# Kernel tuning notes

Hardware: AMD Instinct MI355X
Metric: run time of the kernel (lower is better)

Reference implementation:

```python
import jax, jax.numpy as jnp
import numpy as np

NUM_HEADS = 16

def rotate_half(x):
    h = x.shape[-1] // 2
    return jnp.concatenate([-x[..., h:], x[..., :h]], axis=-1)

def setup_inputs() -> dict:
    key = jax.random.key(0)
    ks = jax.random.split(key, 6)
    B, S, D, HD = 2, 2048, 2048, 128
    x = jax.random.normal(ks[0], (B, S, D), dtype=jnp.float32)
    # rotary tables for positions 0..S-1, per head_dim channel
    inv_freq = 1.0 / (10000.0 ** (jnp.arange(0, HD, 2, dtype=jnp.float32) / HD))
    t = jnp.arange(S, dtype=jnp.float32)
    freqs = jnp.outer(t, inv_freq)              # [S, HD/2]
    emb = jnp.concatenate([freqs, freqs], -1)   # [S, HD]
    cos = jnp.cos(emb)
    sin = jnp.sin(emb)
    scale = 0.02
    qkv_w = jax.random.normal(ks[1], (D, 3 * D), dtype=jnp.float32) * scale
    qkv_b = jnp.zeros((3 * D,), dtype=jnp.float32)
    out_w = jax.random.normal(ks[2], (D, D), dtype=jnp.float32) * scale
    out_b = jnp.zeros((D,), dtype=jnp.float32)
    return {"x": x, "cos": cos, "sin": sin, "qkv_w": qkv_w, "qkv_b": qkv_b,
            "out_w": out_w, "out_b": out_b}

def reference(x, cos, sin, qkv_w, qkv_b, out_w, out_b):
    B, S, D = x.shape
    H = NUM_HEADS
    HD = D // H
    qkv = x @ qkv_w + qkv_b                      # [B,S,3D]
    q, k, v = jnp.split(qkv, 3, axis=-1)
    def to_heads(t):
        return t.reshape(B, S, H, HD).transpose(0, 2, 1, 3)  # [B,H,S,HD]
    q, k, v = to_heads(q), to_heads(k), to_heads(v)
    # RoPE: cos/sin are [S,HD], broadcast over batch/head
    q = q * cos + rotate_half(q) * sin
    k = k * cos + rotate_half(k) * sin
    scores = jnp.einsum('bhqd,bhkd->bhqk', q, k) / jnp.sqrt(jnp.float32(HD))
    causal = jnp.tril(jnp.ones((S, S), dtype=bool))
    scores = jnp.where(causal, scores, jnp.finfo(scores.dtype).min)
    attn = jax.nn.softmax(scores, axis=-1)
    out = jnp.einsum('bhqk,bhkd->bhqd', attn, v)  # [B,H,S,HD]
    out = out.transpose(0, 2, 1, 3).reshape(B, S, D)
    return out @ out_w + out_b
```

## Files before the change

### kernel.cpp

```cpp
#include <hip/hip_runtime.h>
#include <cstddef>
#include <cstdint>

typedef __attribute__((ext_vector_type(8))) short bh8_t;
typedef __attribute__((ext_vector_type(4))) float f4_t;

__device__ __forceinline__ unsigned short f2bf(float x) {
    union { float f; unsigned u; } v; v.f = x;
    unsigned r = v.u + 0x7fffu + ((v.u >> 16) & 1u);
    return (unsigned short)(r >> 16);
}
__device__ __forceinline__ float bf2f(unsigned short u) {
    union { unsigned u; float f; } v; v.u = ((unsigned)u) << 16;
    return v.f;
}

__device__ __forceinline__ void gl_lds16(const void* g, void* l) {
    __builtin_amdgcn_global_load_lds(
        (const __attribute__((address_space(1))) unsigned int*)g,
        (__attribute__((address_space(3))) unsigned int*)l, 16, 0, 0);
}

#define B_    2
#define S_    2048
#define D_    2048
#define H_    16
#define HD_   128

__global__ __launch_bounds__(256) void cvt_f32_bf16(const float* __restrict__ in,
                                                    ushort* __restrict__ out) {
    size_t i = ((size_t)blockIdx.x * 256 + threadIdx.x) * 8;
    float4 a = *(const float4*)&in[i];
    float4 b = *(const float4*)&in[i + 4];
    ushort4 o0, o1;
    o0.x = f2bf(a.x); o0.y = f2bf(a.y); o0.z = f2bf(a.z); o0.w = f2bf(a.w);
    o1.x = f2bf(b.x); o1.y = f2bf(b.y); o1.z = f2bf(b.z); o1.w = f2bf(b.w);
    *(ushort4*)&out[i]     = o0;
    *(ushort4*)&out[i + 4] = o1;
}

__global__ __launch_bounds__(256) void transp_f32_bf16(const float* __restrict__ in,
                                                       ushort* __restrict__ out,
                                                       int R, int C) {
    __shared__ float T[64][68];
    const int t = threadIdx.x, rl = t >> 4, cl = t & 15;
    const int r0 = blockIdx.y * 64, c0 = blockIdx.x * 64;
    #pragma unroll
    for (int j = 0; j < 4; ++j) {
        int row = rl + 16 * j;
        float4 v = *(const float4*)&in[(size_t)(r0 + row) * C + c0 + cl * 4];
        *(float4*)&T[row][cl * 4] = v;
    }
    __syncthreads();
    #pragma unroll
    for (int j = 0; j < 4; ++j) {
        int row = rl + 16 * j;
        ushort4 o;
        o.x = f2bf(T[cl * 4 + 0][row]);
        o.y = f2bf(T[cl * 4 + 1][row]);
        o.z = f2bf(T[cl * 4 + 2][row]);
        o.w = f2bf(T[cl * 4 + 3][row]);
        *(ushort4*)&out[(size_t)(c0 + row) * R + r0 + cl * 4] = o;
    }
}

__global__ __launch_bounds__(256) void qkv_gemm(const ushort* __restrict__ A,
                                                const ushort* __restrict__ Bt,
                                                const float* __restrict__ bias,
                                                ushort* __restrict__ Qb,
                                                ushort* __restrict__ Kb,
                                                ushort* __restrict__ Vtg) {
    __shared__ ushort Al[2][128 * 32];
    __shared__ ushort Bl[2][128 * 32];
    const int tid = threadIdx.x;
    const int l = tid & 63, wv = tid >> 6;
    const int lr = l & 15, bk = l >> 4;
    const int wr = wv >> 1, wc = wv & 1;
    const int row0 = blockIdx.x * 128, col0 = blockIdx.y * 128;

    f4_t zero4 = {0.f, 0.f, 0.f, 0.f};
    f4_t acc[4][4];
    #pragma unroll
    for (int i = 0; i < 4; ++i)
        #pragma unroll
        for (int j = 0; j < 4; ++j) acc[i][j] = zero4;

    const int c0 = tid, c1 = tid + 256;
    const ushort* Ap0 = A  + (size_t)(row0 + (c0 >> 2)) * 2048 + (c0 & 3) * 8;
    const ushort* Ap1 = A  + (size_t)(row0 + (c1 >> 2)) * 2048 + (c1 & 3) * 8;
    const ushort* Bp0 = Bt + (size_t)(col0 + (c0 >> 2)) * 2048 + (c0 & 3) * 8;
    const ushort* Bp1 = Bt + (size_t)(col0 + (c1 >> 2)) * 2048 + (c1 & 3) * 8;
    const int d0 = (c0 - l) * 8, d1 = (c1 - l) * 8;

    auto issue = [&](int k0, int buf) {
        gl_lds16(Ap0 + k0, &Al[buf][d0]);
        gl_lds16(Ap1 + k0, &Al[buf][d1]);
        gl_lds16(Bp0 + k0, &Bl[buf][d0]);
        gl_lds16(Bp1 + k0, &Bl[buf][d1]);
    };

    issue(0, 0);
    for (int k0 = 0; k0 < 2048; k0 += 32) {
        const int buf = (k0 >> 5) & 1;
        if (k0 + 32 < 2048) {
            issue(k0 + 32, buf ^ 1);
            asm volatile("s_waitcnt vmcnt(4)" ::: "memory");
        } else {
            asm volatile("s_waitcnt vmcnt(0)" ::: "memory");
        }
        __builtin_amdgcn_s_barrier();
        asm volatile("" ::: "memory");
        bh8_t af[4], bf[4];
        #pragma unroll
        for (int mf = 0; mf < 4; ++mf)
            af[mf] = *(const bh8_t*)&Al[buf][(wr * 64 + mf * 16 + lr) * 32 + bk * 8];
        #pragma unroll
        for (int nf = 0; nf < 4; ++nf)
            bf[nf] = *(const bh8_t*)&Bl[buf][(wc * 64 + nf * 16 + lr) * 32 + bk * 8];
        __builtin_amdgcn_s_setprio(1);
        #pragma unroll
        for (int mf = 0; mf < 4; ++mf)
            #pragma unroll
            for (int nf = 0; nf < 4; ++nf)
                acc[mf][nf] = __builtin_amdgcn_mfma_f32_16x16x32_bf16(
                    af[mf], bf[nf], acc[mf][nf], 0, 0, 0);
        __builtin_amdgcn_s_setprio(0);
        asm volatile("" ::: "memory");
        __builtin_amdgcn_s_barrier();
        asm volatile("" ::: "memory");
    }

    const int which = col0 >> 11;
    const int h = (col0 & 2047) >> 7;
    if (which < 2) {
        ushort* dst = which == 0 ? Qb : Kb;
        #pragma unroll
        for (int nf = 0; nf < 4; ++nf) {
            int n = col0 + wc * 64 + nf * 16 + lr;
            float bv = bias[n];
            int hd = (n & 2047) & 127;
            #pragma unroll
            for (int mf = 0; mf < 4; ++mf) {
                int mbase = row0 + wr * 64 + mf * 16 + bk * 4;
                #pragma unroll
                for (int r = 0; r < 4; ++r) {
                    int m = mbase + r;
                    int b = m >> 11, s = m & 2047;
                    dst[((size_t)(b * 16 + h) * 2048 + s) * 128 + hd] =
                        f2bf(acc[mf][nf][r] + bv);
                }
            }
        }
    } else {
        #pragma unroll
        for (int nf = 0; nf < 4; ++nf) {
            int n = col0 + wc * 64 + nf * 16 + lr;
            float bv = bias[n];
            int hd = n & 127;
            #pragma unroll
            for (int mf = 0; mf < 4; ++mf) {
                int mbase = row0 + wr * 64 + mf * 16 + bk * 4;
                int b = mbase >> 11, s4 = mbase & 2047;
                int spos = (s4 & ~31) | (((s4 >> 2) & 3) << 3) | (((s4 >> 4) & 1) << 2);
                ushort4 o;
                o.x = f2bf(acc[mf][nf][0] + bv);
                o.y = f2bf(acc[mf][nf][1] + bv);
                o.z = f2bf(acc[mf][nf][2] + bv);
                o.w = f2bf(acc[mf][nf][3] + bv);
                *(ushort4*)&Vtg[((size_t)((b * 16 + h) * 128 + hd)) * 2048 + spos] = o;
            }
        }
    }
}

__global__ __launch_bounds__(256) void rope_bf16(ushort* __restrict__ Qb,
                                                 ushort* __restrict__ Kb,
                                                 const float* __restrict__ cosn,
                                                 const float* __restrict__ sinn) {
    unsigned idx = blockIdx.x * 256 + threadIdx.x;
    int regn = idx >> 20;
    unsigned rest = idx & 1048575u;
    unsigned row = rest >> 4;
    int g = rest & 15;
    int s = row & 2047;
    ushort* base = (regn ? Kb : Qb) + (size_t)row * 128 + g * 4;
    uint2 lo = *(const uint2*)base;
    uint2 hi = *(const uint2*)(base + 64);
    float4 c4 = *(const float4*)&cosn[s * 128 + g * 4];
    float4 s4 = *(const float4*)&sinn[s * 128 + g * 4];
    const float sc = regn ? 1.0f : 0.08838834764831845f;
    const ushort* lp = (const ushort*)&lo;
    const ushort* hp = (const ushort*)&hi;
    float cf[4] = {c4.x, c4.y, c4.z, c4.w};
    float sf[4] = {s4.x, s4.y, s4.z, s4.w};
    ushort4 olo, ohi;
    ushort* olp = (ushort*)&olo;
    ushort* ohp = (ushort*)&ohi;
    #pragma unroll
    for (int e = 0; e < 4; ++e) {
        float lv = bf2f(lp[e]), hv = bf2f(hp[e]);
        olp[e] = f2bf((lv * cf[e] - hv * sf[e]) * sc);
        ohp[e] = f2bf((hv * cf[e] + lv * sf[e]) * sc);
    }
    *(ushort4*)base        = olo;
    *(ushort4*)(base + 64) = ohi;
}

__global__ __launch_bounds__(512) void attn3(const ushort* __restrict__ Qb,
                                             const ushort* __restrict__ Kb,
                                             const ushort* __restrict__ Vtg,
                                             ushort* __restrict__ AO) {
    __shared__ ushort lds[2][16384];
    const int tid = threadIdx.x;
    const int l = tid & 63, wq = tid >> 6;
    const int lr = l & 15, bk = l >> 4;
    const int id = blockIdx.x;
    const int bh = id & 31;
    const int qb2 = 15 - (id >> 5);
    const int q0 = qb2 * 128;
    const int qrow = q0 + wq * 16 + lr;
    const ushort* Qg = Qb + ((size_t)bh * 2048 + qrow) * 128;
    const ushort* KgB = Kb + (size_t)bh * 2048 * 128;
    const ushort* VgB = Vtg + (size_t)bh * 128 * 2048;

    bh8_t qf[4];
    #pragma unroll
    for (int ks = 0; ks < 4; ++ks)
        qf[ks] = *(const bh8_t*)(Qg + ks * 32 + bk * 8);

    float mrun = -1e30f, lrun = 0.f;
    f4_t zero4 = {0.f, 0.f, 0.f, 0.f};
    f4_t oacc[8];
    #pragma unroll
    for (int i = 0; i < 8; ++i) oacc[i] = zero4;

    auto issue = [&](int kt, int buf) {
        ushort* Kl = &lds[buf][0];
        ushort* Vl = &lds[buf][8192];
        const ushort* Kg = KgB + (size_t)kt * 64 * 128;
        #pragma unroll
        for (int i = 0; i < 2; ++i) {
            int c = tid + 512 * i;
            int key = c >> 4, d8 = (c & 15) ^ (key & 7);
            gl_lds16(Kg + key * 128 + d8 * 8, Kl + (size_t)(c - l) * 8);
        }
        #pragma unroll
        for (int i = 0; i < 2; ++i) {
            int c = tid + 512 * i;
            int d = c >> 3, p8 = (c & 7) ^ (d & 7);
            gl_lds16(VgB + (size_t)d * 2048 + kt * 64 + p8 * 8,
                     Vl + (size_t)(c - l) * 8);
        }
    };

    const int nkt = 2 * qb2 + 2;
    issue(0, 0);
    for (int kt = 0; kt < nkt; ++kt) {
        const int buf = kt & 1;
        if (kt + 1 < nkt) {
            issue(kt + 1, buf ^ 1);
            asm volatile("s_waitcnt vmcnt(4)" ::: "memory");
        } else {
            asm volatile("s_waitcnt vmcnt(0)" ::: "memory");
        }
        __builtin_amdgcn_s_barrier();
        asm volatile("" ::: "memory");

        if (kt * 64 <= q0 + wq * 16 + 15) {
            const char* Kl = (const char*)&lds[buf][0];
            const char* Vl = (const char*)&lds[buf][8192];

            f4_t sacc[4];
            #pragma unroll
            for (int kf = 0; kf < 4; ++kf) sacc[kf] = zero4;
            __builtin_amdgcn_s_setprio(1);
            #pragma unroll
            for (int ks = 0; ks < 4; ++ks)
                #pragma unroll
                for (int kf = 0; kf < 4; ++kf) {
                    int key = kf * 16 + lr;
                    int ab = (key * 256 + ks * 64 + bk * 16) ^ ((key & 7) << 4);
                    bh8_t kv = *(const bh8_t*)(Kl + ab);
                    sacc[kf] = __builtin_amdgcn_mfma_f32_16x16x32_bf16(
                        kv, qf[ks], sacc[kf], 0, 0, 0);
                }
            __builtin_amdgcn_s_setprio(0);

            if (kt * 64 + 63 > q0 + wq * 16) {
                #pragma unroll
                for (int kf = 0; kf < 4; ++kf)
                    #pragma unroll
                    for (int r = 0; r < 4; ++r) {
                        int key = kt * 64 + kf * 16 + bk * 4 + r;
                        if (key > qrow) sacc[kf][r] = -1e30f;
                    }
            }
            float mt = -1e30f;
            #pragma unroll
            for (int kf = 0; kf < 4; ++kf)
                #pragma unroll
                for (int r = 0; r < 4; ++r) mt = fmaxf(mt, sacc[kf][r]);
            mt = fmaxf(mt, __shfl_xor(mt, 16));
            mt = fmaxf(mt, __shfl_xor(mt, 32));
            float mnew = fmaxf(mrun, mt);
            float alpha = __expf(mrun - mnew);
            float rsum = 0.f;
            #pragma unroll
            for (int kf = 0; kf < 4; ++kf)
                #pragma unroll
                for (int r = 0; r < 4; ++r) {
                    float p = __expf(sacc[kf][r] - mnew);
                    sacc[kf][r] = p;
                    rsum += p;
                }
            rsum += __shfl_xor(rsum, 16);
            rsum += __shfl_xor(rsum, 32);
            lrun = lrun * alpha + rsum;
            mrun = mnew;
            #pragma unroll
            for (int df = 0; df < 8; ++df) oacc[df] *= alpha;

            union { unsigned u[4]; bh8_t v; } bop[2];
            #pragma unroll
            for (int ks2 = 0; ks2 < 2; ++ks2)
                #pragma unroll
                for (int e = 0; e < 8; e += 2) {
                    unsigned lo16 = f2bf(sacc[2 * ks2 + (e >> 2)][e & 3]);
                    unsigned hi16 = f2bf(sacc[2 * ks2 + ((e + 1) >> 2)][(e + 1) & 3]);
                    bop[ks2].u[e >> 1] = lo16 | (hi16 << 16);
                }
            __builtin_amdgcn_s_setprio(1);
            #pragma unroll
            for (int df = 0; df < 8; ++df) {
                int d = df * 16 + lr;
                #pragma unroll
                for (int ks2 = 0; ks2 < 2; ++ks2) {
                    int ab = (d * 128 + ks2 * 64 + bk * 16) ^ ((d & 7) << 4);
                    bh8_t av = *(const bh8_t*)(Vl + ab);
                    oacc[df] = __builtin_amdgcn_mfma_f32_16x16x32_bf16(
                        av, bop[ks2].v, oacc[df], 0, 0, 0);
                }
            }
            __builtin_amdgcn_s_setprio(0);
        }
        asm volatile("" ::: "memory");
        __builtin_amdgcn_s_barrier();
        asm volatile("" ::: "memory");
    }

    float inv = 1.0f / lrun;
    const int b = bh >> 4, h = bh & 15;
    #pragma unroll
    for (int df = 0; df < 8; ++df) {
        ushort4 o;
        o.x = f2bf(oacc[df][0] * inv);
        o.y = f2bf(oacc[df][1] * inv);
        o.z = f2bf(oacc[df][2] * inv);
        o.w = f2bf(oacc[df][3] * inv);
        size_t off = ((size_t)(b * 2048 + qrow)) * 2048 + h * 128 + df * 16 + bk * 4;
        *(ushort4*)&AO[off] = o;
    }
}

__global__ __launch_bounds__(256) void out_gemm(const ushort* __restrict__ A,
                                                const ushort* __restrict__ Bt,
                                                const float* __restrict__ bias,
                                                float* __restrict__ out) {
    __shared__ ushort Al[2][128 * 32];
    __shared__ ushort Bl[2][128 * 32];
    const int tid = threadIdx.x;
    const int l = tid & 63, wv = tid >> 6;
    const int lr = l & 15, bk = l >> 4;
    const int wr = wv >> 1, wc = wv & 1;
    const int row0 = blockIdx.x * 128, col0 = blockIdx.y * 128;

    f4_t zero4 = {0.f, 0.f, 0.f, 0.f};
    f4_t acc[4][4];
    #pragma unroll
    for (int i = 0; i < 4; ++i)
        #pragma unroll
        for (int j = 0; j < 4; ++j) acc[i][j] = zero4;

    const int c0 = tid, c1 = tid + 256;
    const ushort* Ap0 = A  + (size_t)(row0 + (c0 >> 2)) * 2048 + (c0 & 3) * 8;
    const ushort* Ap1 = A  + (size_t)(row0 + (c1 >> 2)) * 2048 + (c1 & 3) * 8;
    const ushort* Bp0 = Bt + (size_t)(col0 + (c0 >> 2)) * 2048 + (c0 & 3) * 8;
    const ushort* Bp1 = Bt + (size_t)(col0 + (c1 >> 2)) * 2048 + (c1 & 3) * 8;
    const int d0 = (c0 - l) * 8, d1 = (c1 - l) * 8;

    auto issue = [&](int k0, int buf) {
        gl_lds16(Ap0 + k0, &Al[buf][d0]);
        gl_lds16(Ap1 + k0, &Al[buf][d1]);
        gl_lds16(Bp0 + k0, &Bl[buf][d0]);
        gl_lds16(Bp1 + k0, &Bl[buf][d1]);
    };

    issue(0, 0);
    for (int k0 = 0; k0 < 2048; k0 += 32) {
        const int buf = (k0 >> 5) & 1;
        if (k0 + 32 < 2048) {
            issue(k0 + 32, buf ^ 1);
            asm volatile("s_waitcnt vmcnt(4)" ::: "memory");
        } else {
            asm volatile("s_waitcnt vmcnt(0)" ::: "memory");
        }
        __builtin_amdgcn_s_barrier();
        asm volatile("" ::: "memory");
        bh8_t af[4], bf[4];
        #pragma unroll
        for (int mf = 0; mf < 4; ++mf)
            af[mf] = *(const bh8_t*)&Al[buf][(wr * 64 + mf * 16 + lr) * 32 + bk * 8];
        #pragma unroll
        for (int nf = 0; nf < 4; ++nf)
            bf[nf] = *(const bh8_t*)&Bl[buf][(wc * 64 + nf * 16 + lr) * 32 + bk * 8];
        __builtin_amdgcn_s_setprio(1);
        #pragma unroll
        for (int mf = 0; mf < 4; ++mf)
            #pragma unroll
            for (int nf = 0; nf < 4; ++nf)
                acc[mf][nf] = __builtin_amdgcn_mfma_f32_16x16x32_bf16(
                    af[mf], bf[nf], acc[mf][nf], 0, 0, 0);
        __builtin_amdgcn_s_setprio(0);
        asm volatile("" ::: "memory");
        __builtin_amdgcn_s_barrier();
        asm volatile("" ::: "memory");
    }

    #pragma unroll
    for (int nf = 0; nf < 4; ++nf) {
        int n = col0 + wc * 64 + nf * 16 + lr;
        float bv = bias[n];
        #pragma unroll
        for (int mf = 0; mf < 4; ++mf) {
            int mbase = row0 + wr * 64 + mf * 16 + bk * 4;
            #pragma unroll
            for (int r = 0; r < 4; ++r)
                out[(size_t)(mbase + r) * 2048 + n] = acc[mf][nf][r] + bv;
        }
    }
}

extern "C" void kernel_launch(void* const* d_in, const int* in_sizes, int n_in,
                              void* d_out, int out_size, void* d_ws, size_t ws_size,
                              hipStream_t stream)
{
    (void)in_sizes; (void)n_in; (void)out_size; (void)ws_size;
    const float* x     = (const float*)d_in[0];
    const float* cosn  = (const float*)d_in[1];
    const float* sinn  = (const float*)d_in[2];
    const float* qkv_w = (const float*)d_in[3];
    const float* qkv_b = (const float*)d_in[4];
    const float* out_w = (const float*)d_in[5];
    const float* out_b = (const float*)d_in[6];

    char* ws = (char*)d_ws;
    ushort* xb   = (ushort*)(ws);
    ushort* wtb  = (ushort*)(ws + ((size_t)16 << 20));
    ushort* owtb = (ushort*)(ws + ((size_t)40 << 20));
    ushort* Qb   = (ushort*)(ws + ((size_t)48 << 20));
    ushort* Kb   = (ushort*)(ws + ((size_t)64 << 20));
    ushort* Vtg  = (ushort*)(ws + ((size_t)80 << 20));
    ushort* AO   = (ushort*)(ws + ((size_t)96 << 20));

    hipLaunchKernelGGL(cvt_f32_bf16, dim3(4096), dim3(256), 0, stream, x, xb);
    hipLaunchKernelGGL(transp_f32_bf16, dim3(96, 32), dim3(256), 0, stream,
                       qkv_w, wtb, 2048, 6144);
    hipLaunchKernelGGL(transp_f32_bf16, dim3(32, 32), dim3(256), 0, stream,
                       out_w, owtb, 2048, 2048);
    hipLaunchKernelGGL(qkv_gemm, dim3(32, 48), dim3(256), 0, stream,
                       xb, wtb, qkv_b, Qb, Kb, Vtg);
    hipLaunchKernelGGL(rope_bf16, dim3(8192), dim3(256), 0, stream,
                       Qb, Kb, cosn, sinn);
    hipLaunchKernelGGL(attn3, dim3(512), dim3(512), 0, stream,
                       Qb, Kb, Vtg, AO);
    hipLaunchKernelGGL(out_gemm, dim3(32, 16), dim3(256), 0, stream,
                       AO, owtb, out_b, (float*)d_out);
}
```

Measured before the change: 419.5 us.

## Triple-buffer GEMM K-tiles with one barrier per step and rebalance attention block order

Both bf16 GEMMs move from double-buffered to triple-buffered LDS staging. Each step issues the tile two ahead and needs only one barrier instead of two, so global loads get more time to land and the barrier count is halved. The attention kernel now interleaves heavy (late) and light (early) causal query blocks in its launch order, aiming to balance work across waves of blocks. LDS use per GEMM block rises by half, which may reduce occupancy, and with the trailing vmcnt(4) wait the tile t+1 loads must finish before the next iteration reads them.

```diff
diff --git a/kernel.cpp b/kernel.cpp
--- a/kernel.cpp
+++ b/kernel.cpp
@@ -70,8 +70,8 @@
                                                 ushort* __restrict__ Qb,
                                                 ushort* __restrict__ Kb,
                                                 ushort* __restrict__ Vtg) {
-    __shared__ ushort Al[2][128 * 32];
-    __shared__ ushort Bl[2][128 * 32];
+    __shared__ ushort Al[3][128 * 32];
+    __shared__ ushort Bl[3][128 * 32];
     const int tid = threadIdx.x;
     const int l = tid & 63, wv = tid >> 6;
     const int lr = l & 15, bk = l >> 4;
@@ -92,7 +92,8 @@
     const ushort* Bp1 = Bt + (size_t)(col0 + (c1 >> 2)) * 2048 + (c1 & 3) * 8;
     const int d0 = (c0 - l) * 8, d1 = (c1 - l) * 8;
 
-    auto issue = [&](int k0, int buf) {
+    auto issue = [&](int t, int buf) {
+        const int k0 = t * 32;
         gl_lds16(Ap0 + k0, &Al[buf][d0]);
         gl_lds16(Ap1 + k0, &Al[buf][d1]);
         gl_lds16(Bp0 + k0, &Bl[buf][d0]);
@@ -100,16 +101,15 @@
     };
 
     issue(0, 0);
-    for (int k0 = 0; k0 < 2048; k0 += 32) {
-        const int buf = (k0 >> 5) & 1;
-        if (k0 + 32 < 2048) {
-            issue(k0 + 32, buf ^ 1);
-            asm volatile("s_waitcnt vmcnt(4)" ::: "memory");
-        } else {
-            asm volatile("s_waitcnt vmcnt(0)" ::: "memory");
-        }
-        __builtin_amdgcn_s_barrier();
-        asm volatile("" ::: "memory");
+    issue(1, 1);
+    asm volatile("s_waitcnt vmcnt(4)" ::: "memory");
+    __builtin_amdgcn_s_barrier();
+    asm volatile("" ::: "memory");
+
+    for (int t = 0; t < 64; ++t) {
+        const int buf = t % 3;
+        const bool more = (t + 2 < 64);
+        if (more) issue(t + 2, (t + 2) % 3);
         bh8_t af[4], bf[4];
         #pragma unroll
         for (int mf = 0; mf < 4; ++mf)
@@ -125,7 +125,8 @@
                 acc[mf][nf] = __builtin_amdgcn_mfma_f32_16x16x32_bf16(
                     af[mf], bf[nf], acc[mf][nf], 0, 0, 0);
         __builtin_amdgcn_s_setprio(0);
-        asm volatile("" ::: "memory");
+        if (more) asm volatile("s_waitcnt vmcnt(4)" ::: "memory");
+        else      asm volatile("s_waitcnt vmcnt(0)" ::: "memory");
         __builtin_amdgcn_s_barrier();
         asm volatile("" ::: "memory");
     }
@@ -216,7 +217,8 @@
     const int lr = l & 15, bk = l >> 4;
     const int id = blockIdx.x;
     const int bh = id & 31;
-    const int qb2 = 15 - (id >> 5);
+    const int k = id >> 5;
+    const int qb2 = (k < 8) ? 15 - k : k - 8;
     const int q0 = qb2 * 128;
     const int qrow = q0 + wq * 16 + lr;
     const ushort* Qg = Qb + ((size_t)bh * 2048 + qrow) * 128;
@@ -366,8 +368,8 @@
                                                 const ushort* __restrict__ Bt,
                                                 const float* __restrict__ bias,
                                                 float* __restrict__ out) {
-    __shared__ ushort Al[2][128 * 32];
-    __shared__ ushort Bl[2][128 * 32];
+    __shared__ ushort Al[3][128 * 32];
+    __shared__ ushort Bl[3][128 * 32];
     const int tid = threadIdx.x;
     const int l = tid & 63, wv = tid >> 6;
     const int lr = l & 15, bk = l >> 4;
@@ -388,7 +390,8 @@
     const ushort* Bp1 = Bt + (size_t)(col0 + (c1 >> 2)) * 2048 + (c1 & 3) * 8;
     const int d0 = (c0 - l) * 8, d1 = (c1 - l) * 8;
 
-    auto issue = [&](int k0, int buf) {
+    auto issue = [&](int t, int buf) {
+        const int k0 = t * 32;
         gl_lds16(Ap0 + k0, &Al[buf][d0]);
         gl_lds16(Ap1 + k0, &Al[buf][d1]);
         gl_lds16(Bp0 + k0, &Bl[buf][d0]);
@@ -396,16 +399,15 @@
     };
 
     issue(0, 0);
-    for (int k0 = 0; k0 < 2048; k0 += 32) {
-        const int buf = (k0 >> 5) & 1;
-        if (k0 + 32 < 2048) {
-            issue(k0 + 32, buf ^ 1);
-            asm volatile("s_waitcnt vmcnt(4)" ::: "memory");
-        } else {
-            asm volatile("s_waitcnt vmcnt(0)" ::: "memory");
-        }
-        __builtin_amdgcn_s_barrier();
-        asm volatile("" ::: "memory");
+    issue(1, 1);
+    asm volatile("s_waitcnt vmcnt(4)" ::: "memory");
+    __builtin_amdgcn_s_barrier();
+    asm volatile("" ::: "memory");
+
+    for (int t = 0; t < 64; ++t) {
+        const int buf = t % 3;
+        const bool more = (t + 2 < 64);
+        if (more) issue(t + 2, (t + 2) % 3);
         bh8_t af[4], bf[4];
         #pragma unroll
         for (int mf = 0; mf < 4; ++mf)
@@ -421,7 +423,8 @@
                 acc[mf][nf] = __builtin_amdgcn_mfma_f32_16x16x32_bf16(
                     af[mf], bf[nf], acc[mf][nf], 0, 0, 0);
         __builtin_amdgcn_s_setprio(0);
-        asm volatile("" ::: "memory");
+        if (more) asm volatile("s_waitcnt vmcnt(4)" ::: "memory");
+        else      asm volatile("s_waitcnt vmcnt(0)" ::: "memory");
         __builtin_amdgcn_s_barrier();
         asm volatile("" ::: "memory");
     }
```

After: 422.4 us. No clear change (+0.7%).
